# Optimization experiments

Measured on AMD Instinct MI355X. Metric: run time of the kernel, lower is better.

Reference implementation:

```python
import jax, jax.numpy as jnp
import numpy as np

D_MODEL = 256
D_INNER = 512   # expand=2
D_STATE = 16
DT_RANK = 16    # ceil(d_model/16)
D_CONV = 4
N_LAYERS = 2    # per direction
B, N = 2, 1024


def _mamba_layer(x, W_in, cw, cb, W_x, W_dt, b_dt, A_log, Dp, W_out):
    """One mamba_ssm.Mamba forward. x: (B, L, d_model)."""
    Bb, L, _ = x.shape
    xz = x @ W_in.T                        # (B, L, 2*d_inner)
    di = xz.shape[-1] // 2
    xc, z = xz[..., :di], xz[..., di:]
    # causal depthwise conv1d, kernel D_CONV, left-pad d_conv-1
    K = cw.shape[-1]
    xp = jnp.pad(xc, ((0, 0), (K - 1, 0), (0, 0)))
    xc = sum(xp[:, k:k + L, :] * cw[:, k] for k in range(K)) + cb
    xc = jax.nn.silu(xc)
    # input-dependent dt, B, C
    dbl = xc @ W_x.T                       # (B, L, dt_rank + 2*d_state)
    ds = A_log.shape[-1]
    dt = dbl[..., :DT_RANK]
    Bm = dbl[..., DT_RANK:DT_RANK + ds]    # (B, L, d_state)
    Cm = dbl[..., DT_RANK + ds:]           # (B, L, d_state)
    dt = jax.nn.softplus(dt @ W_dt.T + b_dt)  # (B, L, d_inner)
    A = -jnp.exp(A_log)                    # (d_inner, d_state)
    dA = jnp.exp(dt[..., None] * A)                          # (B, L, di, ds)
    dBx = dt[..., None] * Bm[:, :, None, :] * xc[..., None]  # (B, L, di, ds)

    def step(h, inp):
        a_t, b_t, c_t = inp                # (B,di,ds),(B,di,ds),(B,ds)
        h = a_t * h + b_t
        y_t = jnp.einsum('bds,bs->bd', h, c_t)
        return h, y_t

    h0 = jnp.zeros((Bb, di, ds), x.dtype)
    _, ys = jax.lax.scan(step, h0, (dA.transpose(1, 0, 2, 3),
                                    dBx.transpose(1, 0, 2, 3),
                                    Cm.transpose(1, 0, 2)))
    y = ys.transpose(1, 0, 2) + xc * Dp    # skip term D*x
    y = y * jax.nn.silu(z)                 # gate
    return y @ W_out.T                     # (B, L, d_model)


def setup_inputs() -> dict:
    key = jax.random.key(0)
    ks = jax.random.split(key, 10)
    s = 0.05  # weight scale for numerical stability
    nlay = 2 * N_LAYERS  # forward layers then backward layers
    return {
        "x": jax.random.normal(ks[0], (B, N, D_MODEL), jnp.float32),
        "in_proj": jax.random.normal(ks[1], (nlay, 2 * D_INNER, D_MODEL), jnp.float32) * s,
        "conv_w": jax.random.normal(ks[2], (nlay, D_INNER, D_CONV), jnp.float32) * s,
        "conv_b": jax.random.normal(ks[3], (nlay, D_INNER), jnp.float32) * s,
        "x_proj": jax.random.normal(ks[4], (nlay, DT_RANK + 2 * D_STATE, D_INNER), jnp.float32) * s,
        "dt_proj": jax.random.normal(ks[5], (nlay, D_INNER, DT_RANK), jnp.float32) * s,
        "dt_bias": jax.random.normal(ks[6], (nlay, D_INNER), jnp.float32) * s,
        "A_log": jax.random.uniform(ks[7], (nlay, D_INNER, D_STATE), jnp.float32),
        "D": jax.random.uniform(ks[8], (nlay, D_INNER), jnp.float32),
        "out_proj": jax.random.normal(ks[9], (nlay, D_MODEL, D_INNER), jnp.float32) * s,
    }


def reference(x, in_proj, conv_w, conv_b, x_proj, dt_proj, dt_bias, A_log, D, out_proj):
    n = in_proj.shape[0] // 2
    x_fwd = x
    for i in range(n):
        x_fwd = _mamba_layer(x_fwd, in_proj[i], conv_w[i], conv_b[i], x_proj[i],
                             dt_proj[i], dt_bias[i], A_log[i], D[i], out_proj[i])
    x_bwd = x[:, ::-1, :]
    for i in range(n, 2 * n):
        x_bwd = _mamba_layer(x_bwd, in_proj[i], conv_w[i], conv_b[i], x_proj[i],
                             dt_proj[i], dt_bias[i], A_log[i], D[i], out_proj[i])
    x_bwd = x_bwd[:, ::-1, :]
    return jnp.concatenate([x_fwd, x_bwd], axis=-1)  # (B, N, 2*d_model)
```

## Files before the change

### kernel.cpp

```cpp
#include <hip/hip_runtime.h>
#include <math.h>

#define G 2
#define BB 2
#define L 1024
#define DM 256
#define DI 512
#define DS 16
#define DR 16
#define CH 64
#define CL 16
#define RTOT (G*BB*L)
#define SKX 8

typedef short bh8 __attribute__((ext_vector_type(8)));
typedef float f4x __attribute__((ext_vector_type(4)));

__device__ __forceinline__ float silu_f(float x) { return x / (1.f + __expf(-x)); }

__device__ __forceinline__ unsigned short f2bf(float f) {
    unsigned u = __float_as_uint(f);
    unsigned r = u + 0x7FFFu + ((u >> 16) & 1u);
    return (unsigned short)(r >> 16);
}
__device__ __forceinline__ float bf2f(unsigned short s) {
    return __uint_as_float(((unsigned)s) << 16);
}

template<int BM, int SPLITK, int AMAP>
__global__ __launch_bounds__(256) void mfma_gemm(
    const float* __restrict__ A, size_t slabOff, int lda, int Ktot,
    const float* __restrict__ W, int Nout, int step,
    float* __restrict__ C, int ldc, size_t partStride)
{
    constexpr int AP = BM / 32;
    constexpr int CA = BM / 32;
    __shared__ short As_hi[BM * 40];
    __shared__ short As_lo[BM * 40];
    __shared__ short Bs_hi[64 * 40];
    __shared__ short Bs_lo[64 * 40];

    const int row0 = blockIdx.y * BM;
    const int col0 = blockIdx.x * 64;
    const int g    = row0 >> 11;
    const int lay  = g * 2 + step;
    const float* Wg = W + (size_t)lay * Nout * Ktot;
    const int t    = threadIdx.x;
    const int lane = t & 63, wv = t >> 6;
    const int m = lane & 15, quad = lane >> 4;
    const int wr = wv >> 1, wc = wv & 1;

    const int Kc    = Ktot / SPLITK;
    const int kbase = blockIdx.z * Kc;
    const int NT    = Kc / 32;

    float4 pa[CA], pa2[CA], pb[2];
    auto loadT = [&](int kt) {
        const int kb = kbase + kt * 32;
        #pragma unroll
        for (int i = 0; i < CA; i++) {
            int id = t + 256 * i;
            int row = id >> 3, kq = id & 7;
            size_t arow;
            if (AMAP == 1) {
                int gr = row0 + row;
                int gg = gr >> 11, b = (gr >> 10) & 1, l = gr & 1023;
                int sl = gg ? (1023 - l) : l;
                arow = (size_t)(b * 1024 + sl);
            } else {
                arow = (size_t)(row0 + row);
            }
            pa[i] = *(const float4*)&A[arow * lda + kb + kq * 4];
            if (AMAP == 2)
                pa2[i] = *(const float4*)&A[slabOff + arow * lda + kb + kq * 4];
        }
        #pragma unroll
        for (int i = 0; i < 2; i++) {
            int id = t + 256 * i;
            int row = id >> 3, kq = id & 7;
            pb[i] = *(const float4*)&Wg[(size_t)(col0 + row) * Ktot + kb + kq * 4];
        }
    };
    auto cvt_store = [&](short* hi, short* lo, int row, int kq, float4 v) {
        short4 h, l;
        unsigned short s;
        s = f2bf(v.x); h.x = (short)s; l.x = (short)f2bf(v.x - bf2f(s));
        s = f2bf(v.y); h.y = (short)s; l.y = (short)f2bf(v.y - bf2f(s));
        s = f2bf(v.z); h.z = (short)s; l.z = (short)f2bf(v.z - bf2f(s));
        s = f2bf(v.w); h.w = (short)s; l.w = (short)f2bf(v.w - bf2f(s));
        *(short4*)&hi[row * 40 + kq * 4] = h;
        *(short4*)&lo[row * 40 + kq * 4] = l;
    };

    f4x acc[AP][2] = {};
    loadT(0);

    for (int kt = 0; kt < NT; kt++) {
        #pragma unroll
        for (int i = 0; i < CA; i++) {
            int id = t + 256 * i;
            int row = id >> 3, kq = id & 7;
            float4 v = pa[i];
            if (AMAP == 2) { v.x += pa2[i].x; v.y += pa2[i].y; v.z += pa2[i].z; v.w += pa2[i].w; }
            cvt_store(As_hi, As_lo, row, kq, v);
        }
        #pragma unroll
        for (int i = 0; i < 2; i++) {
            int id = t + 256 * i;
            int row = id >> 3, kq = id & 7;
            cvt_store(Bs_hi, Bs_lo, row, kq, pb[i]);
        }
        __syncthreads();
        if (kt + 1 < NT) loadT(kt + 1);

        bh8 ah[AP], al[AP], bh[2], bl[2];
        #pragma unroll
        for (int p = 0; p < AP; p++) {
            int r = wr * (BM / 2) + p * 16 + m;
            ah[p] = *(bh8*)&As_hi[r * 40 + quad * 8];
            al[p] = *(bh8*)&As_lo[r * 40 + quad * 8];
        }
        #pragma unroll
        for (int pb_ = 0; pb_ < 2; pb_++) {
            int r = wc * 32 + pb_ * 16 + m;
            bh[pb_] = *(bh8*)&Bs_hi[r * 40 + quad * 8];
            bl[pb_] = *(bh8*)&Bs_lo[r * 40 + quad * 8];
        }
        #pragma unroll
        for (int p = 0; p < AP; p++)
            #pragma unroll
            for (int q = 0; q < 2; q++) {
                acc[p][q] = __builtin_amdgcn_mfma_f32_16x16x32_bf16(ah[p], bh[q], acc[p][q], 0, 0, 0);
                acc[p][q] = __builtin_amdgcn_mfma_f32_16x16x32_bf16(ah[p], bl[q], acc[p][q], 0, 0, 0);
                acc[p][q] = __builtin_amdgcn_mfma_f32_16x16x32_bf16(al[p], bh[q], acc[p][q], 0, 0, 0);
            }
        __syncthreads();
    }

    float* Cz = C + (size_t)blockIdx.z * partStride;
    #pragma unroll
    for (int p = 0; p < AP; p++)
        #pragma unroll
        for (int q = 0; q < 2; q++) {
            int gcol = col0 + wc * 32 + q * 16 + m;
            #pragma unroll
            for (int r = 0; r < 4; r++) {
                int grow = row0 + wr * (BM / 2) + p * 16 + quad * 4 + r;
                Cz[(size_t)grow * ldc + gcol] = acc[p][q][r];
            }
        }
}

template<int SPLITK>
__global__ __launch_bounds__(256) void gemm64(
    const float* __restrict__ A, int lda, int Ktot,
    const float* __restrict__ W, int Nout, int step,
    float* __restrict__ C, int ldc, size_t partStride)
{
    __shared__ float As[16][68];
    __shared__ float Bs[16][68];

    const int row0 = blockIdx.y * 64;
    const int col0 = blockIdx.x * 64;
    const int g    = row0 >> 11;
    const int lay  = g * 2 + step;
    const float* Wg = W + (size_t)lay * Nout * Ktot;
    const int t  = threadIdx.x;
    const int tx = t & 15, ty = t >> 4;
    const int Kc    = Ktot / SPLITK;
    const int kbase = blockIdx.z * Kc;
    const int NT    = Kc / 16;

    const int sr = t >> 2;
    const int sk = (t & 3) * 4;
    const size_t arow = (size_t)(row0 + sr);
    const bool bok = (col0 + sr < Nout);

    float4 pa, pb;
    auto loadT = [&](int kt) {
        const int kb = kbase + kt * 16 + sk;
        pa = *(const float4*)&A[arow * lda + kb];
        pb = bok ? *(const float4*)&Wg[(size_t)(col0 + sr) * Ktot + kb]
                 : make_float4(0.f, 0.f, 0.f, 0.f);
    };

    float acc[4][4] = {};
    loadT(0);

    for (int kt = 0; kt < NT; kt++) {
        As[sk + 0][sr] = pa.x; As[sk + 1][sr] = pa.y;
        As[sk + 2][sr] = pa.z; As[sk + 3][sr] = pa.w;
        Bs[sk + 0][sr] = pb.x; Bs[sk + 1][sr] = pb.y;
        Bs[sk + 2][sr] = pb.z; Bs[sk + 3][sr] = pb.w;
        __syncthreads();
        if (kt + 1 < NT) loadT(kt + 1);
        #pragma unroll
        for (int kk = 0; kk < 16; kk++) {
            float4 a = *(const float4*)&As[kk][ty * 4];
            float4 b = *(const float4*)&Bs[kk][tx * 4];
            float av[4] = {a.x, a.y, a.z, a.w};
            float bv[4] = {b.x, b.y, b.z, b.w};
            #pragma unroll
            for (int i = 0; i < 4; i++)
                #pragma unroll
                for (int j = 0; j < 4; j++) acc[i][j] += av[i] * bv[j];
        }
        __syncthreads();
    }

    float* Cz = C + (size_t)blockIdx.z * partStride;
    const int col = col0 + tx * 4;
    if (col < Nout) {
        #pragma unroll
        for (int i = 0; i < 4; i++) {
            int r = row0 + ty * 4 + i;
            *(float4*)&Cz[(size_t)r * ldc + col] =
                make_float4(acc[i][0], acc[i][1], acc[i][2], acc[i][3]);
        }
    }
}

__global__ __launch_bounds__(256) void combineOut(
    const float* __restrict__ P, float* __restrict__ out)
{
    int idx = blockIdx.x * 256 + threadIdx.x;
    int c  = idx & 511;
    int bl = idx >> 9;
    int b = bl >> 10, l = bl & 1023;
    int r, col;
    if (c < 256) { r = b * 1024 + l;                 col = c; }
    else         { r = 2048 + b * 1024 + (1023 - l); col = c - 256; }
    size_t o = (size_t)r * 256 + col;
    out[idx] = P[o] + P[(size_t)RTOT * 256 + o];
}

__global__ __launch_bounds__(256) void conv_silu(
    const float* __restrict__ XZ, const float* __restrict__ cw,
    const float* __restrict__ cb, float* __restrict__ XC, int step)
{
    int n = blockIdx.x * 256 + threadIdx.x;
    int d4 = n & 127;
    int r  = n >> 7;
    int g = r >> 11, l = r & 1023;
    int lay = g * 2 + step;
    int d = d4 * 4;
    const float* wb = cw + ((size_t)lay * 512 + d) * 4;
    float4 w0 = *(const float4*)&wb[0];
    float4 w1 = *(const float4*)&wb[4];
    float4 w2 = *(const float4*)&wb[8];
    float4 w3 = *(const float4*)&wb[12];
    float4 acc = *(const float4*)&cb[(size_t)lay * 512 + d];
    #pragma unroll
    for (int k = 0; k < 4; k++) {
        int ls = l - 3 + k;
        if (ls < 0) continue;
        float4 xv = *(const float4*)&XZ[(size_t)(r - 3 + k) * 1024 + d];
        float wk0 = (&w0.x)[k], wk1 = (&w1.x)[k], wk2 = (&w2.x)[k], wk3 = (&w3.x)[k];
        acc.x += wk0 * xv.x; acc.y += wk1 * xv.y;
        acc.z += wk2 * xv.z; acc.w += wk3 * xv.w;
    }
    acc.x = silu_f(acc.x); acc.y = silu_f(acc.y);
    acc.z = silu_f(acc.z); acc.w = silu_f(acc.w);
    *(float4*)&XC[(size_t)r * 512 + d] = acc;
}

__device__ __forceinline__ void stage_dbl(
    float dbl[CL][48], const float* __restrict__ Pdbl, int r0, int tid)
{
    for (int id = tid; id < CL * 48; id += 512) {
        int rr = id / 48, cc = id - rr * 48;
        size_t o = (size_t)(r0 + rr) * 48 + cc;
        float v = 0.f;
        #pragma unroll
        for (int s = 0; s < SKX; s++) v += Pdbl[(size_t)s * (RTOT * 48) + o];
        dbl[rr][cc] = v;
    }
}

__global__ __launch_bounds__(512) void scanA(
    const float* __restrict__ XCb, const float* __restrict__ Pdbl,
    const float* __restrict__ A_log, const float* __restrict__ Wdt,
    const float* __restrict__ bdt,
    float* __restrict__ Aprod, float* __restrict__ Hend, int step)
{
    __shared__ float dbl[CL][48];
    int blk = blockIdx.x;
    int c  = blk & (CH - 1);
    int gb = blk >> 6;
    int g  = gb >> 1;
    int lay = g * 2 + step;
    int d = threadIdx.x;
    int r0 = gb * L + c * CL;

    stage_dbl(dbl, Pdbl, r0, threadIdx.x);

    float wdt[16];
    const float* wrow = Wdt + ((size_t)lay * DI + d) * DR;
    #pragma unroll
    for (int k = 0; k < 16; k += 4) {
        float4 v = *(const float4*)&wrow[k];
        wdt[k] = v.x; wdt[k + 1] = v.y; wdt[k + 2] = v.z; wdt[k + 3] = v.w;
    }
    float bias = bdt[(size_t)lay * DI + d];

    float a[DS], h[DS], ap[DS];
    const float* al = A_log + ((size_t)lay * DI + d) * DS;
    #pragma unroll
    for (int s = 0; s < DS; s++) { a[s] = -__expf(al[s]); h[s] = 0.f; ap[s] = 1.f; }
    __syncthreads();

    for (int tt = 0; tt < CL; tt++) {
        float dtr = bias;
        #pragma unroll
        for (int k = 0; k < 16; k++) dtr += dbl[tt][k] * wdt[k];
        float dt = (dtr > 20.f) ? dtr : log1pf(__expf(dtr));
        float xc = XCb[(size_t)(r0 + tt) * DI + d];
        float dx = dt * xc;
        #pragma unroll
        for (int s = 0; s < DS; s++) {
            float da = __expf(dt * a[s]);
            h[s] = da * h[s] + dx * dbl[tt][16 + s];
            ap[s] *= da;
        }
    }
    size_t base = ((size_t)(gb * DI + d) * CH + c) * DS;
    #pragma unroll
    for (int q = 0; q < 4; q++) {
        *(float4*)&Aprod[base + q * 4] = make_float4(ap[q*4], ap[q*4+1], ap[q*4+2], ap[q*4+3]);
        *(float4*)&Hend [base + q * 4] = make_float4(h[q*4],  h[q*4+1],  h[q*4+2],  h[q*4+3]);
    }
}

__global__ __launch_bounds__(256) void scanCombine(
    const float* __restrict__ Aprod, const float* __restrict__ Hend,
    float* __restrict__ Hinit)
{
    int idx = blockIdx.x * 256 + threadIdx.x;
    int s  = idx & 15;
    int gd = idx >> 4;
    size_t base = (size_t)gd * CH * DS + s;
    float h = 0.f;
    for (int c0 = 0; c0 < CH; c0 += 8) {
        float ap[8], e[8];
        #pragma unroll
        for (int j = 0; j < 8; j++) {
            size_t o = base + (size_t)(c0 + j) * DS;
            ap[j] = Aprod[o]; e[j] = Hend[o];
        }
        #pragma unroll
        for (int j = 0; j < 8; j++) {
            Hinit[base + (size_t)(c0 + j) * DS] = h;
            h = ap[j] * h + e[j];
        }
    }
}

__global__ __launch_bounds__(512) void scanB(
    const float* __restrict__ XCb, const float* __restrict__ Pdbl,
    const float* __restrict__ XZ, const float* __restrict__ A_log,
    const float* __restrict__ Wdt, const float* __restrict__ bdt,
    const float* __restrict__ Dp, const float* __restrict__ Hinit,
    float* __restrict__ Yb, int step)
{
    __shared__ float dbl[CL][48];
    int blk = blockIdx.x;
    int c  = blk & (CH - 1);
    int gb = blk >> 6;
    int g  = gb >> 1;
    int lay = g * 2 + step;
    int d = threadIdx.x;
    int r0 = gb * L + c * CL;

    stage_dbl(dbl, Pdbl, r0, threadIdx.x);

    float wdt[16];
    const float* wrow = Wdt + ((size_t)lay * DI + d) * DR;
    #pragma unroll
    for (int k = 0; k < 16; k += 4) {
        float4 v = *(const float4*)&wrow[k];
        wdt[k] = v.x; wdt[k + 1] = v.y; wdt[k + 2] = v.z; wdt[k + 3] = v.w;
    }
    float bias = bdt[(size_t)lay * DI + d];

    float a[DS], h[DS];
    const float* al = A_log + ((size_t)lay * DI + d) * DS;
    size_t base = ((size_t)(gb * DI + d) * CH + c) * DS;
    #pragma unroll
    for (int s = 0; s < DS; s++) { a[s] = -__expf(al[s]); h[s] = Hinit[base + s]; }
    float Dv = Dp[(size_t)lay * DI + d];
    __syncthreads();

    for (int tt = 0; tt < CL; tt++) {
        int r = r0 + tt;
        float dtr = bias;
        #pragma unroll
        for (int k = 0; k < 16; k++) dtr += dbl[tt][k] * wdt[k];
        float dt = (dtr > 20.f) ? dtr : log1pf(__expf(dtr));
        float xc = XCb[(size_t)r * DI + d];
        float dx = dt * xc;
        float y = 0.f;
        #pragma unroll
        for (int s = 0; s < DS; s++) {
            float da = __expf(dt * a[s]);
            h[s] = da * h[s] + dx * dbl[tt][16 + s];
            y += h[s] * dbl[tt][32 + s];
        }
        y += xc * Dv;
        float z = XZ[(size_t)r * 1024 + 512 + d];
        y *= silu_f(z);
        Yb[(size_t)r * DI + d] = y;
    }
}

extern "C" void kernel_launch(void* const* d_in, const int* in_sizes, int n_in,
                              void* d_out, int out_size, void* d_ws, size_t ws_size,
                              hipStream_t stream)
{
    const float* x        = (const float*)d_in[0];
    const float* in_proj  = (const float*)d_in[1];
    const float* conv_w   = (const float*)d_in[2];
    const float* conv_b   = (const float*)d_in[3];
    const float* x_proj   = (const float*)d_in[4];
    const float* dt_proj  = (const float*)d_in[5];
    const float* dt_bias  = (const float*)d_in[6];
    const float* A_log    = (const float*)d_in[7];
    const float* Dp       = (const float*)d_in[8];
    const float* out_proj = (const float*)d_in[9];
    float* out = (float*)d_out;

    float* w = (float*)d_ws;
    size_t o = 0;
    float* XZ    = w + o; o += (size_t)RTOT * 1024;
    float* XCb   = w + o; o += (size_t)RTOT * DI;
    float* Yb    = w + o; o += (size_t)RTOT * DI;
    float* Pdbl  = w + o; o += (size_t)SKX * RTOT * 48;
    float* Aprod = w + o; o += (size_t)G * BB * DI * CH * DS;
    float* Hend  = w + o; o += (size_t)G * BB * DI * CH * DS;
    float* Hinit = w + o; o += (size_t)G * BB * DI * CH * DS;
    float* Pout  = w + o; o += (size_t)2 * RTOT * DM;
    (void)ws_size; (void)in_sizes; (void)n_in; (void)out_size;

    for (int step = 0; step < 2; step++) {
        if (step == 0)
            mfma_gemm<128, 1, 1><<<dim3(16, 32, 1), 256, 0, stream>>>(
                x, 0, DM, DM, in_proj, 2 * DI, 0, XZ, 1024, 0);
        else
            mfma_gemm<128, 1, 2><<<dim3(16, 32, 1), 256, 0, stream>>>(
                Pout, (size_t)RTOT * DM, DM, DM, in_proj, 2 * DI, 1, XZ, 1024, 0);
        conv_silu<<<RTOT * 128 / 256, 256, 0, stream>>>(XZ, conv_w, conv_b, XCb, step);
        gemm64<SKX><<<dim3(1, 64, SKX), 256, 0, stream>>>(
            XCb, DI, DI, x_proj, 48, step, Pdbl, 48, (size_t)RTOT * 48);
        scanA<<<G * BB * CH, 512, 0, stream>>>(
            XCb, Pdbl, A_log, dt_proj, dt_bias, Aprod, Hend, step);
        scanCombine<<<(G * BB * DI * DS) / 256, 256, 0, stream>>>(Aprod, Hend, Hinit);
        scanB<<<G * BB * CH, 512, 0, stream>>>(
            XCb, Pdbl, XZ, A_log, dt_proj, dt_bias, Dp, Hinit, Yb, step);
        mfma_gemm<64, 2, 0><<<dim3(4, 64, 2), 256, 0, stream>>>(
            Yb, 0, DI, DI, out_proj, DM, step, Pout, DM, (size_t)RTOT * DM);
    }
    combineOut<<<(2 * 1024 * 512) / 256, 256, 0, stream>>>(Pout, out);
}
```

Before: 270.2 us.

## Fuse conv into x_proj GEMM, merge scan stages cooperatively, drop combine kernel

The causal conv plus SiLU is now computed inside the x_proj GEMM's A-tile load, which also writes XCb, so the separate conv_silu kernel is removed. scanA, scanCombine and scanB become one cooperative kernel that uses grid-wide syncs. It keeps dt and xc in registers, so the second pass no longer recomputes them or restages dbl. The final out_proj GEMM of the last step writes straight into the output layout (including the reversed backward half) without split-K, which removes combineOut. The trade-offs are fewer launches and less global traffic against extra register pressure, the cost of grid barriers, and a cooperative launch that requires all 256 blocks to be resident at once.

```diff
diff --git a/kernel.cpp b/kernel.cpp
--- a/kernel.cpp
+++ b/kernel.cpp
@@ -1,5 +1,8 @@
 #include <hip/hip_runtime.h>
+#include <hip/hip_cooperative_groups.h>
 #include <math.h>
+
+namespace cg = cooperative_groups;
 
 #define G 2
 #define BB 2
@@ -27,7 +30,7 @@
     return __uint_as_float(((unsigned)s) << 16);
 }
 
-template<int BM, int SPLITK, int AMAP>
+template<int BM, int SPLITK, int AMAP, int CMODE>
 __global__ __launch_bounds__(256) void mfma_gemm(
     const float* __restrict__ A, size_t slabOff, int lda, int Ktot,
     const float* __restrict__ W, int Nout, int step,
@@ -146,22 +149,31 @@
             #pragma unroll
             for (int r = 0; r < 4; r++) {
                 int grow = row0 + wr * (BM / 2) + p * 16 + quad * 4 + r;
-                Cz[(size_t)grow * ldc + gcol] = acc[p][q][r];
+                if (CMODE == 2) {
+                    int b = (grow >> 10) & 1, l = grow & 1023;
+                    size_t dst = (g == 0)
+                        ? ((size_t)(b * 1024 + l) * 512 + gcol)
+                        : ((size_t)(b * 1024 + (1023 - l)) * 512 + 256 + gcol);
+                    C[dst] = acc[p][q][r];
+                } else {
+                    Cz[(size_t)grow * ldc + gcol] = acc[p][q][r];
+                }
             }
         }
 }
 
 template<int SPLITK>
-__global__ __launch_bounds__(256) void gemm64(
-    const float* __restrict__ A, int lda, int Ktot,
-    const float* __restrict__ W, int Nout, int step,
-    float* __restrict__ C, int ldc, size_t partStride)
+__global__ __launch_bounds__(256) void gemm_xproj(
+    const float* __restrict__ XZ, const float* __restrict__ cw,
+    const float* __restrict__ cb, float* __restrict__ XCb,
+    const float* __restrict__ W, int step,
+    float* __restrict__ C, size_t partStride)
 {
+    constexpr int Nout = 48, Ktot = DI;
     __shared__ float As[16][68];
     __shared__ float Bs[16][68];
 
     const int row0 = blockIdx.y * 64;
-    const int col0 = blockIdx.x * 64;
     const int g    = row0 >> 11;
     const int lay  = g * 2 + step;
     const float* Wg = W + (size_t)lay * Nout * Ktot;
@@ -173,14 +185,31 @@
 
     const int sr = t >> 2;
     const int sk = (t & 3) * 4;
-    const size_t arow = (size_t)(row0 + sr);
-    const bool bok = (col0 + sr < Nout);
+    const int gr = row0 + sr;
+    const int l  = gr & 1023;
+    const bool bok = (sr < Nout);
 
     float4 pa, pb;
     auto loadT = [&](int kt) {
-        const int kb = kbase + kt * 16 + sk;
-        pa = *(const float4*)&A[arow * lda + kb];
-        pb = bok ? *(const float4*)&Wg[(size_t)(col0 + sr) * Ktot + kb]
+        const int ch = kbase + kt * 16 + sk;
+        const float* wb = cw + ((size_t)lay * 512 + ch) * 4;
+        float4 w0 = *(const float4*)&wb[0];
+        float4 w1 = *(const float4*)&wb[4];
+        float4 w2 = *(const float4*)&wb[8];
+        float4 w3 = *(const float4*)&wb[12];
+        float4 acc = *(const float4*)&cb[(size_t)lay * 512 + ch];
+        #pragma unroll
+        for (int k = 0; k < 4; k++) {
+            if (l - 3 + k < 0) continue;
+            float4 xv = *(const float4*)&XZ[(size_t)(gr - 3 + k) * 1024 + ch];
+            acc.x += (&w0.x)[k] * xv.x; acc.y += (&w1.x)[k] * xv.y;
+            acc.z += (&w2.x)[k] * xv.z; acc.w += (&w3.x)[k] * xv.w;
+        }
+        acc.x = silu_f(acc.x); acc.y = silu_f(acc.y);
+        acc.z = silu_f(acc.z); acc.w = silu_f(acc.w);
+        pa = acc;
+        *(float4*)&XCb[(size_t)gr * 512 + ch] = acc;
+        pb = bok ? *(const float4*)&Wg[(size_t)sr * Ktot + kbase + kt * 16 + sk]
                  : make_float4(0.f, 0.f, 0.f, 0.f);
     };
 
@@ -209,65 +238,36 @@
     }
 
     float* Cz = C + (size_t)blockIdx.z * partStride;
-    const int col = col0 + tx * 4;
+    const int col = tx * 4;
     if (col < Nout) {
         #pragma unroll
         for (int i = 0; i < 4; i++) {
             int r = row0 + ty * 4 + i;
-            *(float4*)&Cz[(size_t)r * ldc + col] =
+            *(float4*)&Cz[(size_t)r * 48 + col] =
                 make_float4(acc[i][0], acc[i][1], acc[i][2], acc[i][3]);
         }
     }
 }
 
-__global__ __launch_bounds__(256) void combineOut(
-    const float* __restrict__ P, float* __restrict__ out)
+__global__ __launch_bounds__(512) void scanFused(
+    const float* __restrict__ XCb, const float* __restrict__ Pdbl,
+    const float* __restrict__ XZ, const float* __restrict__ A_log,
+    const float* __restrict__ Wdt, const float* __restrict__ bdt,
+    const float* __restrict__ Dp,
+    float* __restrict__ Aprod, float* __restrict__ Hend,
+    float* __restrict__ Hinit, float* __restrict__ Yb, int step)
 {
-    int idx = blockIdx.x * 256 + threadIdx.x;
-    int c  = idx & 511;
-    int bl = idx >> 9;
-    int b = bl >> 10, l = bl & 1023;
-    int r, col;
-    if (c < 256) { r = b * 1024 + l;                 col = c; }
-    else         { r = 2048 + b * 1024 + (1023 - l); col = c - 256; }
-    size_t o = (size_t)r * 256 + col;
-    out[idx] = P[o] + P[(size_t)RTOT * 256 + o];
-}
-
-__global__ __launch_bounds__(256) void conv_silu(
-    const float* __restrict__ XZ, const float* __restrict__ cw,
-    const float* __restrict__ cb, float* __restrict__ XC, int step)
-{
-    int n = blockIdx.x * 256 + threadIdx.x;
-    int d4 = n & 127;
-    int r  = n >> 7;
-    int g = r >> 11, l = r & 1023;
-    int lay = g * 2 + step;
-    int d = d4 * 4;
-    const float* wb = cw + ((size_t)lay * 512 + d) * 4;
-    float4 w0 = *(const float4*)&wb[0];
-    float4 w1 = *(const float4*)&wb[4];
-    float4 w2 = *(const float4*)&wb[8];
-    float4 w3 = *(const float4*)&wb[12];
-    float4 acc = *(const float4*)&cb[(size_t)lay * 512 + d];
-    #pragma unroll
-    for (int k = 0; k < 4; k++) {
-        int ls = l - 3 + k;
-        if (ls < 0) continue;
-        float4 xv = *(const float4*)&XZ[(size_t)(r - 3 + k) * 1024 + d];
-        float wk0 = (&w0.x)[k], wk1 = (&w1.x)[k], wk2 = (&w2.x)[k], wk3 = (&w3.x)[k];
-        acc.x += wk0 * xv.x; acc.y += wk1 * xv.y;
-        acc.z += wk2 * xv.z; acc.w += wk3 * xv.w;
-    }
-    acc.x = silu_f(acc.x); acc.y = silu_f(acc.y);
-    acc.z = silu_f(acc.z); acc.w = silu_f(acc.w);
-    *(float4*)&XC[(size_t)r * 512 + d] = acc;
-}
-
-__device__ __forceinline__ void stage_dbl(
-    float dbl[CL][48], const float* __restrict__ Pdbl, int r0, int tid)
-{
-    for (int id = tid; id < CL * 48; id += 512) {
+    cg::grid_group gridg = cg::this_grid();
+    __shared__ float dbl[CL][48];
+    const int blk = blockIdx.x;
+    const int c  = blk & (CH - 1);
+    const int gb = blk >> 6;
+    const int g  = gb >> 1;
+    const int lay = g * 2 + step;
+    const int d = threadIdx.x;
+    const int r0 = gb * L + c * CL;
+
+    for (int id = threadIdx.x; id < CL * 48; id += 512) {
         int rr = id / 48, cc = id - rr * 48;
         size_t o = (size_t)(r0 + rr) * 48 + cc;
         float v = 0.f;
@@ -275,24 +275,6 @@
         for (int s = 0; s < SKX; s++) v += Pdbl[(size_t)s * (RTOT * 48) + o];
         dbl[rr][cc] = v;
     }
-}
-
-__global__ __launch_bounds__(512) void scanA(
-    const float* __restrict__ XCb, const float* __restrict__ Pdbl,
-    const float* __restrict__ A_log, const float* __restrict__ Wdt,
-    const float* __restrict__ bdt,
-    float* __restrict__ Aprod, float* __restrict__ Hend, int step)
-{
-    __shared__ float dbl[CL][48];
-    int blk = blockIdx.x;
-    int c  = blk & (CH - 1);
-    int gb = blk >> 6;
-    int g  = gb >> 1;
-    int lay = g * 2 + step;
-    int d = threadIdx.x;
-    int r0 = gb * L + c * CL;
-
-    stage_dbl(dbl, Pdbl, r0, threadIdx.x);
 
     float wdt[16];
     const float* wrow = Wdt + ((size_t)lay * DI + d) * DR;
@@ -301,9 +283,9 @@
         float4 v = *(const float4*)&wrow[k];
         wdt[k] = v.x; wdt[k + 1] = v.y; wdt[k + 2] = v.z; wdt[k + 3] = v.w;
     }
-    float bias = bdt[(size_t)lay * DI + d];
-
-    float a[DS], h[DS], ap[DS];
+    const float bias = bdt[(size_t)lay * DI + d];
+
+    float a[DS], h[DS], ap[DS], dt[CL], xc[CL];
     const float* al = A_log + ((size_t)lay * DI + d) * DS;
     #pragma unroll
     for (int s = 0; s < DS; s++) { a[s] = -__expf(al[s]); h[s] = 0.f; ap[s] = 1.f; }
@@ -313,102 +295,64 @@
         float dtr = bias;
         #pragma unroll
         for (int k = 0; k < 16; k++) dtr += dbl[tt][k] * wdt[k];
-        float dt = (dtr > 20.f) ? dtr : log1pf(__expf(dtr));
-        float xc = XCb[(size_t)(r0 + tt) * DI + d];
-        float dx = dt * xc;
+        dt[tt] = (dtr > 20.f) ? dtr : log1pf(__expf(dtr));
+        xc[tt] = XCb[(size_t)(r0 + tt) * DI + d];
+        float dx = dt[tt] * xc[tt];
         #pragma unroll
         for (int s = 0; s < DS; s++) {
-            float da = __expf(dt * a[s]);
+            float da = __expf(dt[tt] * a[s]);
             h[s] = da * h[s] + dx * dbl[tt][16 + s];
             ap[s] *= da;
         }
     }
-    size_t base = ((size_t)(gb * DI + d) * CH + c) * DS;
+    const size_t base = ((size_t)(gb * DI + d) * CH + c) * DS;
     #pragma unroll
     for (int q = 0; q < 4; q++) {
         *(float4*)&Aprod[base + q * 4] = make_float4(ap[q*4], ap[q*4+1], ap[q*4+2], ap[q*4+3]);
         *(float4*)&Hend [base + q * 4] = make_float4(h[q*4],  h[q*4+1],  h[q*4+2],  h[q*4+3]);
     }
-}
-
-__global__ __launch_bounds__(256) void scanCombine(
-    const float* __restrict__ Aprod, const float* __restrict__ Hend,
-    float* __restrict__ Hinit)
-{
-    int idx = blockIdx.x * 256 + threadIdx.x;
-    int s  = idx & 15;
-    int gd = idx >> 4;
-    size_t base = (size_t)gd * CH * DS + s;
-    float h = 0.f;
-    for (int c0 = 0; c0 < CH; c0 += 8) {
-        float ap[8], e[8];
-        #pragma unroll
-        for (int j = 0; j < 8; j++) {
-            size_t o = base + (size_t)(c0 + j) * DS;
-            ap[j] = Aprod[o]; e[j] = Hend[o];
-        }
-        #pragma unroll
-        for (int j = 0; j < 8; j++) {
-            Hinit[base + (size_t)(c0 + j) * DS] = h;
-            h = ap[j] * h + e[j];
-        }
-    }
-}
-
-__global__ __launch_bounds__(512) void scanB(
-    const float* __restrict__ XCb, const float* __restrict__ Pdbl,
-    const float* __restrict__ XZ, const float* __restrict__ A_log,
-    const float* __restrict__ Wdt, const float* __restrict__ bdt,
-    const float* __restrict__ Dp, const float* __restrict__ Hinit,
-    float* __restrict__ Yb, int step)
-{
-    __shared__ float dbl[CL][48];
-    int blk = blockIdx.x;
-    int c  = blk & (CH - 1);
-    int gb = blk >> 6;
-    int g  = gb >> 1;
-    int lay = g * 2 + step;
-    int d = threadIdx.x;
-    int r0 = gb * L + c * CL;
-
-    stage_dbl(dbl, Pdbl, r0, threadIdx.x);
-
-    float wdt[16];
-    const float* wrow = Wdt + ((size_t)lay * DI + d) * DR;
+    __threadfence();
+    gridg.sync();
+
+    if (blk < 64) {
+        int idx = blk * 512 + threadIdx.x;
+        int s  = idx & 15;
+        int gd = idx >> 4;
+        size_t cb_ = (size_t)gd * CH * DS + s;
+        float hh = 0.f;
+        for (int c0 = 0; c0 < CH; c0 += 8) {
+            float apv[8], e[8];
+            #pragma unroll
+            for (int j = 0; j < 8; j++) {
+                size_t o = cb_ + (size_t)(c0 + j) * DS;
+                apv[j] = Aprod[o]; e[j] = Hend[o];
+            }
+            #pragma unroll
+            for (int j = 0; j < 8; j++) {
+                Hinit[cb_ + (size_t)(c0 + j) * DS] = hh;
+                hh = apv[j] * hh + e[j];
+            }
+        }
+    }
+    __threadfence();
+    gridg.sync();
+
     #pragma unroll
-    for (int k = 0; k < 16; k += 4) {
-        float4 v = *(const float4*)&wrow[k];
-        wdt[k] = v.x; wdt[k + 1] = v.y; wdt[k + 2] = v.z; wdt[k + 3] = v.w;
-    }
-    float bias = bdt[(size_t)lay * DI + d];
-
-    float a[DS], h[DS];
-    const float* al = A_log + ((size_t)lay * DI + d) * DS;
-    size_t base = ((size_t)(gb * DI + d) * CH + c) * DS;
-    #pragma unroll
-    for (int s = 0; s < DS; s++) { a[s] = -__expf(al[s]); h[s] = Hinit[base + s]; }
-    float Dv = Dp[(size_t)lay * DI + d];
-    __syncthreads();
-
+    for (int s = 0; s < DS; s++) h[s] = Hinit[base + s];
+    const float Dv = Dp[(size_t)lay * DI + d];
     for (int tt = 0; tt < CL; tt++) {
-        int r = r0 + tt;
-        float dtr = bias;
-        #pragma unroll
-        for (int k = 0; k < 16; k++) dtr += dbl[tt][k] * wdt[k];
-        float dt = (dtr > 20.f) ? dtr : log1pf(__expf(dtr));
-        float xc = XCb[(size_t)r * DI + d];
-        float dx = dt * xc;
+        float dx = dt[tt] * xc[tt];
         float y = 0.f;
         #pragma unroll
         for (int s = 0; s < DS; s++) {
-            float da = __expf(dt * a[s]);
+            float da = __expf(dt[tt] * a[s]);
             h[s] = da * h[s] + dx * dbl[tt][16 + s];
             y += h[s] * dbl[tt][32 + s];
         }
-        y += xc * Dv;
-        float z = XZ[(size_t)r * 1024 + 512 + d];
+        y += xc[tt] * Dv;
+        float z = XZ[(size_t)(r0 + tt) * 1024 + 512 + d];
         y *= silu_f(z);
-        Yb[(size_t)r * DI + d] = y;
+        Yb[(size_t)(r0 + tt) * DI + d] = y;
     }
 }
 
@@ -442,21 +386,31 @@
 
     for (int step = 0; step < 2; step++) {
         if (step == 0)
-            mfma_gemm<128, 1, 1><<<dim3(16, 32, 1), 256, 0, stream>>>(
+            mfma_gemm<128, 1, 1, 0><<<dim3(16, 32, 1), 256, 0, stream>>>(
                 x, 0, DM, DM, in_proj, 2 * DI, 0, XZ, 1024, 0);
         else
-            mfma_gemm<128, 1, 2><<<dim3(16, 32, 1), 256, 0, stream>>>(
+            mfma_gemm<128, 1, 2, 0><<<dim3(16, 32, 1), 256, 0, stream>>>(
                 Pout, (size_t)RTOT * DM, DM, DM, in_proj, 2 * DI, 1, XZ, 1024, 0);
-        conv_silu<<<RTOT * 128 / 256, 256, 0, stream>>>(XZ, conv_w, conv_b, XCb, step);
-        gemm64<SKX><<<dim3(1, 64, SKX), 256, 0, stream>>>(
-            XCb, DI, DI, x_proj, 48, step, Pdbl, 48, (size_t)RTOT * 48);
-        scanA<<<G * BB * CH, 512, 0, stream>>>(
-            XCb, Pdbl, A_log, dt_proj, dt_bias, Aprod, Hend, step);
-        scanCombine<<<(G * BB * DI * DS) / 256, 256, 0, stream>>>(Aprod, Hend, Hinit);
-        scanB<<<G * BB * CH, 512, 0, stream>>>(
-            XCb, Pdbl, XZ, A_log, dt_proj, dt_bias, Dp, Hinit, Yb, step);
-        mfma_gemm<64, 2, 0><<<dim3(4, 64, 2), 256, 0, stream>>>(
-            Yb, 0, DI, DI, out_proj, DM, step, Pout, DM, (size_t)RTOT * DM);
-    }
-    combineOut<<<(2 * 1024 * 512) / 256, 256, 0, stream>>>(Pout, out);
-}
+
+        gemm_xproj<SKX><<<dim3(1, 64, SKX), 256, 0, stream>>>(
+            XZ, conv_w, conv_b, XCb, x_proj, step, Pdbl, (size_t)RTOT * 48);
+
+        {
+            const float* a0 = XCb;  const float* a1 = Pdbl; const float* a2 = XZ;
+            const float* a3 = A_log; const float* a4 = dt_proj; const float* a5 = dt_bias;
+            const float* a6 = Dp;
+            float* a7 = Aprod; float* a8 = Hend; float* a9 = Hinit; float* a10 = Yb;
+            int a11 = step;
+            void* sargs[] = {&a0, &a1, &a2, &a3, &a4, &a5, &a6, &a7, &a8, &a9, &a10, &a11};
+            hipLaunchCooperativeKernel((const void*)scanFused,
+                                       dim3(G * BB * CH), dim3(512), sargs, 0, stream);
+        }
+
+        if (step == 0)
+            mfma_gemm<64, 2, 0, 0><<<dim3(4, 64, 2), 256, 0, stream>>>(
+                Yb, 0, DI, DI, out_proj, DM, 0, Pout, DM, (size_t)RTOT * DM);
+        else
+            mfma_gemm<64, 1, 0, 2><<<dim3(4, 64, 1), 256, 0, stream>>>(
+                Yb, 0, DI, DI, out_proj, DM, 1, out, DM, 0);
+    }
+}
```

Result: slower. 678.8 us (+151.2%).

## Fuse conv+SiLU into x_proj GEMM and write final output directly from out_proj GEMM

Applied to the files above, without the earlier changes.

The causal depthwise conv and SiLU are now computed inside the x_proj GEMM's A-tile loader, which also writes XCb for later kernels, so the separate conv_silu kernel launch is removed. The last out_proj GEMM drops split-K and scatters results straight into the final concatenated, direction-reversed output layout, removing the combineOut kernel. Step 0 still uses split-K with two partial slabs in Pout, and step 1's in_proj GEMM reads Pout with AMAP=2, which presumably sums them. Each split-K slice of the x_proj GEMM recomputes conv only for its own K range, so no work is duplicated. Risks are a lower-parallelism out_proj GEMM in step 1 (half the blocks) and scattered stores.

```diff
diff --git a/kernel.cpp b/kernel.cpp
--- a/kernel.cpp
+++ b/kernel.cpp
@@ -27,7 +27,7 @@
     return __uint_as_float(((unsigned)s) << 16);
 }
 
-template<int BM, int SPLITK, int AMAP>
+template<int BM, int SPLITK, int AMAP, int CMODE>
 __global__ __launch_bounds__(256) void mfma_gemm(
     const float* __restrict__ A, size_t slabOff, int lda, int Ktot,
     const float* __restrict__ W, int Nout, int step,
@@ -146,22 +146,31 @@
             #pragma unroll
             for (int r = 0; r < 4; r++) {
                 int grow = row0 + wr * (BM / 2) + p * 16 + quad * 4 + r;
-                Cz[(size_t)grow * ldc + gcol] = acc[p][q][r];
+                if (CMODE == 2) {
+                    int b = (grow >> 10) & 1, l = grow & 1023;
+                    size_t dst = (g == 0)
+                        ? ((size_t)(b * 1024 + l) * 512 + gcol)
+                        : ((size_t)(b * 1024 + (1023 - l)) * 512 + 256 + gcol);
+                    C[dst] = acc[p][q][r];
+                } else {
+                    Cz[(size_t)grow * ldc + gcol] = acc[p][q][r];
+                }
             }
         }
 }
 
 template<int SPLITK>
-__global__ __launch_bounds__(256) void gemm64(
-    const float* __restrict__ A, int lda, int Ktot,
-    const float* __restrict__ W, int Nout, int step,
-    float* __restrict__ C, int ldc, size_t partStride)
-{
+__global__ __launch_bounds__(256) void gemm_xproj(
+    const float* __restrict__ XZ, const float* __restrict__ cw,
+    const float* __restrict__ cb, float* __restrict__ XCb,
+    const float* __restrict__ W, int step,
+    float* __restrict__ C, size_t partStride)
+{
+    constexpr int Nout = 48, Ktot = DI;
     __shared__ float As[16][68];
     __shared__ float Bs[16][68];
 
     const int row0 = blockIdx.y * 64;
-    const int col0 = blockIdx.x * 64;
     const int g    = row0 >> 11;
     const int lay  = g * 2 + step;
     const float* Wg = W + (size_t)lay * Nout * Ktot;
@@ -173,14 +182,31 @@
 
     const int sr = t >> 2;
     const int sk = (t & 3) * 4;
-    const size_t arow = (size_t)(row0 + sr);
-    const bool bok = (col0 + sr < Nout);
+    const int gr = row0 + sr;
+    const int l  = gr & 1023;
+    const bool bok = (sr < Nout);
 
     float4 pa, pb;
     auto loadT = [&](int kt) {
-        const int kb = kbase + kt * 16 + sk;
-        pa = *(const float4*)&A[arow * lda + kb];
-        pb = bok ? *(const float4*)&Wg[(size_t)(col0 + sr) * Ktot + kb]
+        const int ch = kbase + kt * 16 + sk;
+        const float* wb = cw + ((size_t)lay * 512 + ch) * 4;
+        float4 w0 = *(const float4*)&wb[0];
+        float4 w1 = *(const float4*)&wb[4];
+        float4 w2 = *(const float4*)&wb[8];
+        float4 w3 = *(const float4*)&wb[12];
+        float4 acc = *(const float4*)&cb[(size_t)lay * 512 + ch];
+        #pragma unroll
+        for (int k = 0; k < 4; k++) {
+            if (l - 3 + k < 0) continue;
+            float4 xv = *(const float4*)&XZ[(size_t)(gr - 3 + k) * 1024 + ch];
+            acc.x += (&w0.x)[k] * xv.x; acc.y += (&w1.x)[k] * xv.y;
+            acc.z += (&w2.x)[k] * xv.z; acc.w += (&w3.x)[k] * xv.w;
+        }
+        acc.x = silu_f(acc.x); acc.y = silu_f(acc.y);
+        acc.z = silu_f(acc.z); acc.w = silu_f(acc.w);
+        pa = acc;
+        *(float4*)&XCb[(size_t)gr * 512 + ch] = acc;
+        pb = bok ? *(const float4*)&Wg[(size_t)sr * Ktot + kbase + kt * 16 + sk]
                  : make_float4(0.f, 0.f, 0.f, 0.f);
     };
 
@@ -209,59 +235,15 @@
     }
 
     float* Cz = C + (size_t)blockIdx.z * partStride;
-    const int col = col0 + tx * 4;
+    const int col = tx * 4;
     if (col < Nout) {
         #pragma unroll
         for (int i = 0; i < 4; i++) {
             int r = row0 + ty * 4 + i;
-            *(float4*)&Cz[(size_t)r * ldc + col] =
+            *(float4*)&Cz[(size_t)r * 48 + col] =
                 make_float4(acc[i][0], acc[i][1], acc[i][2], acc[i][3]);
         }
     }
-}
-
-__global__ __launch_bounds__(256) void combineOut(
-    const float* __restrict__ P, float* __restrict__ out)
-{
-    int idx = blockIdx.x * 256 + threadIdx.x;
-    int c  = idx & 511;
-    int bl = idx >> 9;
-    int b = bl >> 10, l = bl & 1023;
-    int r, col;
-    if (c < 256) { r = b * 1024 + l;                 col = c; }
-    else         { r = 2048 + b * 1024 + (1023 - l); col = c - 256; }
-    size_t o = (size_t)r * 256 + col;
-    out[idx] = P[o] + P[(size_t)RTOT * 256 + o];
-}
-
-__global__ __launch_bounds__(256) void conv_silu(
-    const float* __restrict__ XZ, const float* __restrict__ cw,
-    const float* __restrict__ cb, float* __restrict__ XC, int step)
-{
-    int n = blockIdx.x * 256 + threadIdx.x;
-    int d4 = n & 127;
-    int r  = n >> 7;
-    int g = r >> 11, l = r & 1023;
-    int lay = g * 2 + step;
-    int d = d4 * 4;
-    const float* wb = cw + ((size_t)lay * 512 + d) * 4;
-    float4 w0 = *(const float4*)&wb[0];
-    float4 w1 = *(const float4*)&wb[4];
-    float4 w2 = *(const float4*)&wb[8];
-    float4 w3 = *(const float4*)&wb[12];
-    float4 acc = *(const float4*)&cb[(size_t)lay * 512 + d];
-    #pragma unroll
-    for (int k = 0; k < 4; k++) {
-        int ls = l - 3 + k;
-        if (ls < 0) continue;
-        float4 xv = *(const float4*)&XZ[(size_t)(r - 3 + k) * 1024 + d];
-        float wk0 = (&w0.x)[k], wk1 = (&w1.x)[k], wk2 = (&w2.x)[k], wk3 = (&w3.x)[k];
-        acc.x += wk0 * xv.x; acc.y += wk1 * xv.y;
-        acc.z += wk2 * xv.z; acc.w += wk3 * xv.w;
-    }
-    acc.x = silu_f(acc.x); acc.y = silu_f(acc.y);
-    acc.z = silu_f(acc.z); acc.w = silu_f(acc.w);
-    *(float4*)&XC[(size_t)r * 512 + d] = acc;
 }
 
 __device__ __forceinline__ void stage_dbl(
@@ -442,21 +424,26 @@
 
     for (int step = 0; step < 2; step++) {
         if (step == 0)
-            mfma_gemm<128, 1, 1><<<dim3(16, 32, 1), 256, 0, stream>>>(
+            mfma_gemm<128, 1, 1, 0><<<dim3(16, 32, 1), 256, 0, stream>>>(
                 x, 0, DM, DM, in_proj, 2 * DI, 0, XZ, 1024, 0);
         else
-            mfma_gemm<128, 1, 2><<<dim3(16, 32, 1), 256, 0, stream>>>(
+            mfma_gemm<128, 1, 2, 0><<<dim3(16, 32, 1), 256, 0, stream>>>(
                 Pout, (size_t)RTOT * DM, DM, DM, in_proj, 2 * DI, 1, XZ, 1024, 0);
-        conv_silu<<<RTOT * 128 / 256, 256, 0, stream>>>(XZ, conv_w, conv_b, XCb, step);
-        gemm64<SKX><<<dim3(1, 64, SKX), 256, 0, stream>>>(
-            XCb, DI, DI, x_proj, 48, step, Pdbl, 48, (size_t)RTOT * 48);
+
+        gemm_xproj<SKX><<<dim3(1, 64, SKX), 256, 0, stream>>>(
+            XZ, conv_w, conv_b, XCb, x_proj, step, Pdbl, (size_t)RTOT * 48);
+
         scanA<<<G * BB * CH, 512, 0, stream>>>(
             XCb, Pdbl, A_log, dt_proj, dt_bias, Aprod, Hend, step);
         scanCombine<<<(G * BB * DI * DS) / 256, 256, 0, stream>>>(Aprod, Hend, Hinit);
         scanB<<<G * BB * CH, 512, 0, stream>>>(
             XCb, Pdbl, XZ, A_log, dt_proj, dt_bias, Dp, Hinit, Yb, step);
-        mfma_gemm<64, 2, 0><<<dim3(4, 64, 2), 256, 0, stream>>>(
-            Yb, 0, DI, DI, out_proj, DM, step, Pout, DM, (size_t)RTOT * DM);
-    }
-    combineOut<<<(2 * 1024 * 512) / 256, 256, 0, stream>>>(Pout, out);
-}
+
+        if (step == 0)
+            mfma_gemm<64, 2, 0, 0><<<dim3(4, 64, 2), 256, 0, stream>>>(
+                Yb, 0, DI, DI, out_proj, DM, 0, Pout, DM, (size_t)RTOT * DM);
+        else
+            mfma_gemm<64, 1, 0, 2><<<dim3(4, 64, 1), 256, 0, stream>>>(
+                Yb, 0, DI, DI, out_proj, DM, 1, out, DM, 0);
+    }
+}
```

Measured after the change: 266.3 us. Within noise of the previous version (-1.4%).
